# Performance work log

Hardware: AMD Instinct MI355X
Metric: run time of the kernel (lower is better)

The kernel has to match this reference:

```python
import jax, jax.numpy as jnp
import numpy as np

B, C, H, W = 8, 512, 32, 32
NH = 8
DH = C // NH
HW = H * W
LN_EPS = 1e-5
NORM_EPS = 1e-12  # torch F.normalize eps


def setup_inputs() -> dict:
    key = jax.random.key(0)
    ks = jax.random.split(key, 8)
    s = 0.02
    return {
        "x": jax.random.normal(ks[0], (B, C, H, W), dtype=jnp.float32),
        "qkv_w": jax.random.normal(ks[1], (3 * C, C), dtype=jnp.float32) * s,
        "proj_w": jax.random.normal(ks[2], (C, C), dtype=jnp.float32) * s,
        "proj_b": jnp.zeros((C,), dtype=jnp.float32),
        "temperature": jnp.ones((NH, 1, 1), dtype=jnp.float32),
        "ln_g": jnp.ones((C,), dtype=jnp.float32),
        "ln_b": jnp.zeros((C,), dtype=jnp.float32),
        "pos_embed": jax.random.normal(ks[3], (1, HW, C), dtype=jnp.float32) * s,
        "dw_w": jax.random.normal(ks[4], (C, 1, 3, 3), dtype=jnp.float32) * s,
        "dw_b": jnp.zeros((C,), dtype=jnp.float32),
        "pw_w": jax.random.normal(ks[5], (C, C, 1, 1), dtype=jnp.float32) * s,
        "pw_b": jnp.zeros((C,), dtype=jnp.float32),
    }


def _l2norm_tokens(t):
    # normalize along token axis (dim=-2), like F.normalize(t, dim=-2)
    n = jnp.sqrt(jnp.sum(t * t, axis=-2, keepdims=True))
    return t / jnp.maximum(n, NORM_EPS)


def _layernorm(t, g, b):
    mu = jnp.mean(t, axis=-1, keepdims=True)
    var = jnp.mean((t - mu) ** 2, axis=-1, keepdims=True)
    return (t - mu) * jax.lax.rsqrt(var + LN_EPS) * g + b


def _dsconv(t, dw_w, dw_b, pw_w, pw_b):
    # depthwise 3x3 SAME + pointwise 1x1, NCHW / OIHW
    y = jax.lax.conv_general_dilated(
        t, dw_w, window_strides=(1, 1), padding="SAME",
        dimension_numbers=("NCHW", "OIHW", "NCHW"), feature_group_count=C)
    y = y + dw_b[None, :, None, None]
    y = jax.lax.conv_general_dilated(
        y, pw_w, window_strides=(1, 1), padding="SAME",
        dimension_numbers=("NCHW", "OIHW", "NCHW"))
    return y + pw_b[None, :, None, None]


def reference(x, qkv_w, proj_w, proj_b, temperature, ln_g, ln_b, pos_embed, dw_w, dw_b, pw_w, pw_b):
    save = x
    t = jnp.transpose(x.reshape(B, C, HW), (0, 2, 1))  # [B, HW, C]
    t = t + pos_embed
    # qkv projection (no bias)
    qkv = t @ qkv_w.T  # [B, HW, 3C]
    qkv = qkv.reshape(B, HW, 3, NH, DH).transpose(2, 0, 3, 1, 4)  # [3,B,NH,HW,DH]
    q, k, v = qkv[0], qkv[1], qkv[2]
    q = _l2norm_tokens(q)
    k = _l2norm_tokens(k)
    attn = jnp.einsum("bhnd,bhmd->bhnm", q, k) * temperature[None]  # [B,NH,HW,HW]
    attn = jax.nn.softmax(attn, axis=-1)
    o = jnp.einsum("bhnm,bhmd->bhnd", attn, v)  # [B,NH,HW,DH]
    o = o.transpose(0, 2, 1, 3).reshape(B, HW, C)
    o = o @ proj_w.T + proj_b
    o = _layernorm(o, ln_g, ln_b)
    o = jnp.transpose(o, (0, 2, 1)).reshape(B, C, H, W)
    o = o + save
    return o + _dsconv(o, dw_w, dw_b, pw_w, pw_b)
```

## Files before the change

kernel.cpp:

```cpp
#include <hip/hip_runtime.h>
#include <math.h>

#define BB_ 8
#define C_ 512
#define C3_ 1536
#define HW_ 1024
#define NH_ 8
#define DH_ 64
#define HH_ 32
#define WW_ 32

typedef __attribute__((ext_vector_type(8))) short short8;
typedef __attribute__((ext_vector_type(4))) short short4v;
typedef __attribute__((ext_vector_type(8))) unsigned short ushort8;
typedef __attribute__((ext_vector_type(4))) unsigned short ushort4_t;
typedef __attribute__((ext_vector_type(4))) float f32x4;
typedef unsigned short ushort;

__device__ inline ushort f2bf(float f) {
  union { float f; unsigned u; } v;
  v.f = f;
  unsigned r = v.u + 0x7fffu + ((v.u >> 16) & 1u);
  return (ushort)(r >> 16);
}
__device__ inline float bf2f(ushort u) {
  union { unsigned u; float f; } v;
  v.u = ((unsigned)u) << 16;
  return v.f;
}

#define GLD16(gptr, lptr)                                                     \
  __builtin_amdgcn_global_load_lds(                                           \
      (const __attribute__((address_space(1))) unsigned int*)(gptr),          \
      (__attribute__((address_space(3))) unsigned int*)(lptr), 16, 0, 0)

__device__ inline f32x4 pv_mfma(const ushort* vp, short4v pf, f32x4 acc) {
#if __has_builtin(__builtin_amdgcn_mfma_f32_16x16x16_bf16)
  short4v vf = *(const short4v*)vp;
  return __builtin_amdgcn_mfma_f32_16x16x16_bf16(vf, pf, acc, 0, 0, 0);
#elif __has_builtin(__builtin_amdgcn_mfma_f32_16x16x16bf16_1k)
  short4v vf = *(const short4v*)vp;
  return __builtin_amdgcn_mfma_f32_16x16x16bf16_1k(vf, pf, acc, 0, 0, 0);
#else
  short4v v4 = *(const short4v*)vp;
  short8 vf = {v4[0], v4[1], v4[2], v4[3], 0, 0, 0, 0};
  short8 pf8 = {pf[0], pf[1], pf[2], pf[3], 0, 0, 0, 0};
  return __builtin_amdgcn_mfma_f32_16x16x32_bf16(vf, pf8, acc, 0, 0, 0);
#endif
}

__global__ void cvt_weights_kernel(const float* __restrict__ qkv_w,
                                   const float* __restrict__ proj_w,
                                   const float* __restrict__ pw_w,
                                   ushort* __restrict__ dst) {
  int i = blockIdx.x * 256 + threadIdx.x;
  if (i < 786432) dst[i] = f2bf(qkv_w[i]);
  else if (i < 1048576) dst[i] = f2bf(proj_w[i - 786432]);
  else dst[i] = f2bf(pw_w[i - 1048576]);
}

__global__ __launch_bounds__(256) void add_pos_kernel(
    const float* __restrict__ x, const float* __restrict__ pos,
    ushort* __restrict__ t, ushort* __restrict__ xT) {
  __shared__ float tile[64][65];
  const int tid = threadIdx.x;
  const int n0 = blockIdx.x * 64, c0 = blockIdx.y * 64, b = blockIdx.z;
#pragma unroll
  for (int it = 0; it < 4; it++) {
    int c_l = (tid >> 4) + it * 16;
    int n_l4 = (tid & 15) * 4;
    float4 v = *(const float4*)&x[((size_t)(b * C_ + c0 + c_l)) * HW_ + n0 + n_l4];
    tile[c_l][n_l4 + 0] = v.x;
    tile[c_l][n_l4 + 1] = v.y;
    tile[c_l][n_l4 + 2] = v.z;
    tile[c_l][n_l4 + 3] = v.w;
  }
  __syncthreads();
#pragma unroll
  for (int it = 0; it < 4; it++) {
    int n_l = (tid >> 4) + it * 16;
    int c_l4 = (tid & 15) * 4;
    size_t token = (size_t)(b * HW_ + n0 + n_l);
    float4 pv = *(const float4*)&pos[(n0 + n_l) * C_ + c0 + c_l4];
    float xv0 = tile[c_l4 + 0][n_l], xv1 = tile[c_l4 + 1][n_l];
    float xv2 = tile[c_l4 + 2][n_l], xv3 = tile[c_l4 + 3][n_l];
    ushort4_t tb = {f2bf(xv0 + pv.x), f2bf(xv1 + pv.y), f2bf(xv2 + pv.z),
                    f2bf(xv3 + pv.w)};
    ushort4_t xb = {f2bf(xv0), f2bf(xv1), f2bf(xv2), f2bf(xv3)};
    *(ushort4_t*)&t[token * C_ + c0 + c_l4] = tb;
    *(ushort4_t*)&xT[token * C_ + c0 + c_l4] = xb;
  }
}

__global__ __launch_bounds__(256) void gemm_128(
    const ushort* __restrict__ A, const ushort* __restrict__ Wm,
    ushort* __restrict__ out, int N, int K) {
  __shared__ alignas(16) ushort As[128 * 32];
  __shared__ alignas(16) ushort Bs[128 * 32];
  const int bn = blockIdx.x * 128, bm = blockIdx.y * 128;
  const int tid = threadIdx.x;
  const int w = tid >> 6, lane = tid & 63;
  const int wm = 64 * (w & 1), wn = 64 * (w >> 1);
  const int l15 = lane & 15, lq = lane >> 4;

  f32x4 acc[4][4];
#pragma unroll
  for (int i = 0; i < 4; i++)
#pragma unroll
    for (int j = 0; j < 4; j++) acc[i][j] = (f32x4){0.f, 0.f, 0.f, 0.f};

  const int srr = lane >> 2, sq1 = lane & 3;

  for (int k0 = 0; k0 < K; k0 += 32) {
    __syncthreads();
#pragma unroll
    for (int j = 0; j < 2; j++) {
      int r = 32 * w + 16 * j + srr;
      int q = (sq1 - (r >> 1)) & 3;
      GLD16(A + (size_t)(bm + r) * K + k0 + q * 8, &As[(32 * w + 16 * j) * 32]);
      GLD16(Wm + (size_t)(bn + r) * K + k0 + q * 8, &Bs[(32 * w + 16 * j) * 32]);
    }
    __syncthreads();
    short8 af[4], bf[4];
#pragma unroll
    for (int nt = 0; nt < 4; nt++) {
      int r = wm + nt * 16 + l15;
      af[nt] = *(const short8*)&As[r * 32 + (((lq + (r >> 1)) & 3) * 8)];
      int c = wn + nt * 16 + l15;
      bf[nt] = *(const short8*)&Bs[c * 32 + (((lq + (c >> 1)) & 3) * 8)];
    }
#pragma unroll
    for (int i = 0; i < 4; i++)
#pragma unroll
      for (int j = 0; j < 4; j++)
        acc[i][j] = __builtin_amdgcn_mfma_f32_16x16x32_bf16(af[i], bf[j],
                                                            acc[i][j], 0, 0, 0);
  }

#pragma unroll
  for (int i = 0; i < 4; i++) {
#pragma unroll
    for (int j = 0; j < 4; j++) {
      int c = bn + wn + j * 16 + l15;
#pragma unroll
      for (int r = 0; r < 4; r++) {
        int m = bm + wm + i * 16 + lq * 4 + r;
        out[(size_t)m * N + c] = f2bf(acc[i][j][r]);
      }
    }
  }
}

template <int EPI>
__global__ __launch_bounds__(256) void gemm_n64(
    const ushort* __restrict__ A, const ushort* __restrict__ Wm,
    const float* __restrict__ bias, float* __restrict__ out,
    const float* __restrict__ resid, int N, int K) {
  __shared__ alignas(16) ushort As[128 * 32];
  __shared__ alignas(16) ushort Bs[64 * 32];
  const int bn = blockIdx.x * 64, bm = blockIdx.y * 128;
  const int tid = threadIdx.x;
  const int w = tid >> 6, lane = tid & 63;
  const int wm = 64 * (w & 1), wn = 32 * (w >> 1);
  const int l15 = lane & 15, lq = lane >> 4;

  f32x4 acc[4][2];
#pragma unroll
  for (int i = 0; i < 4; i++)
#pragma unroll
    for (int j = 0; j < 2; j++) acc[i][j] = (f32x4){0.f, 0.f, 0.f, 0.f};

  const int srr = lane >> 2, sq1 = lane & 3;

  for (int k0 = 0; k0 < K; k0 += 32) {
    __syncthreads();
#pragma unroll
    for (int j = 0; j < 2; j++) {
      int r = 32 * w + 16 * j + srr;
      int q = (sq1 - (r >> 1)) & 3;
      GLD16(A + (size_t)(bm + r) * K + k0 + q * 8, &As[(32 * w + 16 * j) * 32]);
    }
    {
      int r = 16 * w + srr;
      int q = (sq1 - (r >> 1)) & 3;
      GLD16(Wm + (size_t)(bn + r) * K + k0 + q * 8, &Bs[(16 * w) * 32]);
    }
    __syncthreads();
    short8 af[4], bf[2];
#pragma unroll
    for (int nt = 0; nt < 4; nt++) {
      int r = wm + nt * 16 + l15;
      af[nt] = *(const short8*)&As[r * 32 + (((lq + (r >> 1)) & 3) * 8)];
    }
#pragma unroll
    for (int j = 0; j < 2; j++) {
      int c = wn + j * 16 + l15;
      bf[j] = *(const short8*)&Bs[c * 32 + (((lq + (c >> 1)) & 3) * 8)];
    }
#pragma unroll
    for (int i = 0; i < 4; i++)
#pragma unroll
      for (int j = 0; j < 2; j++)
        acc[i][j] = __builtin_amdgcn_mfma_f32_16x16x32_bf16(af[i], bf[j],
                                                            acc[i][j], 0, 0, 0);
  }

#pragma unroll
  for (int i = 0; i < 4; i++) {
#pragma unroll
    for (int j = 0; j < 2; j++) {
      int c = bn + wn + j * 16 + l15;
      float bv = bias[c];
#pragma unroll
      for (int r = 0; r < 4; r++) {
        int m = bm + wm + i * 16 + lq * 4 + r;
        float v = acc[i][j][r] + bv;
        if (EPI == 1) {
          out[(size_t)m * N + c] = v;
        } else {
          int b = m >> 10, s = m & (HW_ - 1);
          out[((size_t)(b * C_ + c)) * HW_ + s] = v + resid[(size_t)m * C_ + c];
        }
      }
    }
  }
}

__global__ __launch_bounds__(256) void vt_kernel(const ushort* __restrict__ qkv,
                                                 ushort* __restrict__ vt) {
  __shared__ ushort tileT[64][72];
  const int bh = blockIdx.x >> 2, seg = blockIdx.x & 3;
  const int b = bh >> 3, h = bh & 7;
  const int tid = threadIdx.x;
  const ushort* src = qkv + (size_t)b * HW_ * C3_ + 2 * C_ + h * 64;
  for (int t = 0; t < 4; t++) {
    int n0 = seg * 256 + t * 64;
    __syncthreads();
#pragma unroll
    for (int it = 0; it < 2; it++) {
      int row = it * 32 + (tid >> 3);
      int c8 = (tid & 7) * 8;
      ushort8 v = *(const ushort8*)&src[(size_t)(n0 + row) * C3_ + c8];
#pragma unroll
      for (int j = 0; j < 8; j++) tileT[c8 + j][row] = v[j];
    }
    __syncthreads();
#pragma unroll
    for (int it = 0; it < 2; it++) {
      int d = it * 32 + (tid >> 3);
      int nch = (tid & 7) * 8;
      ushort8 o8 = *(const ushort8*)&tileT[d][nch];
      *(ushort8*)&vt[((size_t)(bh * 64 + d)) * HW_ + n0 + nch] = o8;
    }
  }
}

__global__ __launch_bounds__(256) void qk_norms_stage1(
    const ushort* __restrict__ qkv, float* __restrict__ partials) {
  __shared__ float smq[32][65], smk[32][65];
  const int blk = blockIdx.x;
  const int bh = blk >> 3, seg = blk & 7;
  const int b = bh >> 3, h = bh & 7;
  const int tid = threadIdx.x;
  const int trow = tid >> 3, chunk = tid & 7;
  float sq[8] = {}, sk[8] = {};
  const ushort* base = qkv + (size_t)b * HW_ * C3_ + h * 64 + chunk * 8;
#pragma unroll
  for (int i = 0; i < 4; i++) {
    int n = seg * 128 + i * 32 + trow;
    const ushort* p = base + (size_t)n * C3_;
    ushort8 q8 = *(const ushort8*)p;
    ushort8 k8 = *(const ushort8*)(p + C_);
#pragma unroll
    for (int j = 0; j < 8; j++) {
      float qv = bf2f(q8[j]), kv = bf2f(k8[j]);
      sq[j] += qv * qv;
      sk[j] += kv * kv;
    }
  }
#pragma unroll
  for (int j = 0; j < 8; j++) {
    smq[trow][chunk * 8 + j] = sq[j];
    smk[trow][chunk * 8 + j] = sk[j];
  }
  __syncthreads();
  if (tid < 64) {
    float s = 0.f;
    for (int i = 0; i < 32; i++) s += smq[i][tid];
    partials[((size_t)(bh * 8 + seg) * 2 + 0) * 64 + tid] = s;
  } else if (tid < 128) {
    int d = tid - 64;
    float s = 0.f;
    for (int i = 0; i < 32; i++) s += smk[i][d];
    partials[((size_t)(bh * 8 + seg) * 2 + 1) * 64 + d] = s;
  }
}

__global__ void qk_norms_stage2(const float* __restrict__ partials,
                                float* __restrict__ invq,
                                float* __restrict__ invk) {
  const int bh = blockIdx.x;
  const int tid = threadIdx.x;
  const int which = tid >> 6, d = tid & 63;
  float s = 0.f;
#pragma unroll
  for (int seg = 0; seg < 8; seg++)
    s += partials[((size_t)(bh * 8 + seg) * 2 + which) * 64 + d];
  float r = 1.0f / fmaxf(sqrtf(s), 1e-12f);
  if (which == 0) invq[bh * 64 + d] = r;
  else invk[bh * 64 + d] = r;
}

__global__ __launch_bounds__(512) void attn_mfma_kernel(
    const ushort* __restrict__ qkv, const ushort* __restrict__ vt,
    const float* __restrict__ invq, const float* __restrict__ invk,
    const float* __restrict__ temp, ushort* __restrict__ o) {
  __shared__ alignas(16) ushort Ks[64 * 64];
  __shared__ alignas(16) ushort Vts[64 * 64];

  const int tid = threadIdx.x;
  const int w = tid >> 6, lane = tid & 63;
  const int quad = lane >> 4, lcol = lane & 15;
  const int bh = blockIdx.x >> 3;
  const int qt = blockIdx.x & 7;
  const int b = bh >> 3, h = bh & 7;
  const int q0 = qt * 128;

  short8 qf[2];
  {
    const int m = q0 + w * 16 + lcol;
    const ushort* qrow = qkv + ((size_t)(b * HW_ + m)) * C3_ + h * 64;
    const float tmp = temp[h];
#pragma unroll
    for (int kc = 0; kc < 2; kc++) {
      union { short8 v; ushort u[8]; } pk;
#pragma unroll
      for (int j = 0; j < 8; j++) {
        int d = kc * 32 + quad * 8 + j;
        float s = invq[bh * 64 + d] * invk[bh * 64 + d] * tmp;
        pk.u[j] = f2bf(bf2f(qrow[d]) * s);
      }
      qf[kc] = pk.v;
    }
  }

  f32x4 ot[4];
#pragma unroll
  for (int dt = 0; dt < 4; dt++) ot[dt] = (f32x4){0.f, 0.f, 0.f, 0.f};
  float lsum = 0.f;

  const ushort* kg = qkv + (size_t)b * HW_ * C3_ + C_ + h * 64;
  const ushort* vg = vt + (size_t)(bh * 64) * HW_;

  const int srow = tid >> 3;
  const int sc = tid & 7;
  const int scg = sc ^ (srow & 7);

  for (int kt = 0; kt < 16; kt++) {
    __syncthreads();
    GLD16(kg + (size_t)(kt * 64 + srow) * C3_ + scg * 8, &Ks[w * 512]);
    GLD16(vg + (size_t)srow * HW_ + kt * 64 + scg * 8, &Vts[w * 512]);
    __syncthreads();

    f32x4 sfr[4];
#pragma unroll
    for (int nt = 0; nt < 4; nt++) sfr[nt] = (f32x4){0.f, 0.f, 0.f, 0.f};
#pragma unroll
    for (int kc = 0; kc < 2; kc++) {
#pragma unroll
      for (int nt = 0; nt < 4; nt++) {
        int row = nt * 16 + lcol;
        short8 kf = *(const short8*)
            &Ks[row * 64 + (((kc * 4 + quad) ^ (row & 7)) * 8)];
        sfr[nt] =
            __builtin_amdgcn_mfma_f32_16x16x32_bf16(kf, qf[kc], sfr[nt], 0, 0, 0);
      }
    }

    ushort pk[4][4];
#pragma unroll
    for (int nt = 0; nt < 4; nt++) {
#pragma unroll
      for (int r = 0; r < 4; r++) {
        float e = __expf(sfr[nt][r]);
        lsum += e;
        pk[nt][r] = f2bf(e);
      }
    }

#pragma unroll
    for (int nt = 0; nt < 4; nt++) {
      short4v pf = {(short)pk[nt][0], (short)pk[nt][1], (short)pk[nt][2],
                    (short)pk[nt][3]};
      int key = nt * 16 + quad * 4;
#pragma unroll
      for (int dt = 0; dt < 4; dt++) {
        int d = dt * 16 + lcol;
        const ushort* vp =
            &Vts[d * 64 + (((key >> 3) ^ (d & 7)) * 8) + (key & 7)];
        ot[dt] = pv_mfma(vp, pf, ot[dt]);
      }
    }
  }

  lsum += __shfl_xor(lsum, 16);
  lsum += __shfl_xor(lsum, 32);
  const float inv = 1.0f / lsum;

  const int m = q0 + w * 16 + lcol;
  ushort* orow = o + ((size_t)(b * HW_ + m)) * C_ + h * 64;
#pragma unroll
  for (int dt = 0; dt < 4; dt++) {
    ushort4_t pkb = {f2bf(ot[dt][0] * inv), f2bf(ot[dt][1] * inv),
                     f2bf(ot[dt][2] * inv), f2bf(ot[dt][3] * inv)};
    *(ushort4_t*)&orow[dt * 16 + quad * 4] = pkb;
  }
}

__global__ void ln_residual_kernel(float* __restrict__ po, const ushort* xT,
                                   const float* __restrict__ g,
                                   const float* __restrict__ bb, ushort* ybf) {
  int token = blockIdx.x;
  int t = threadIdx.x;
  float* row = po + (size_t)token * C_;
  float v0 = row[t], v1 = row[t + 256];
  float s = v0 + v1;
#pragma unroll
  for (int off = 32; off; off >>= 1) s += __shfl_xor(s, off);
  __shared__ float wr[4];
  if ((t & 63) == 0) wr[t >> 6] = s;
  __syncthreads();
  float mu = (wr[0] + wr[1] + wr[2] + wr[3]) * (1.0f / C_);
  float d0 = v0 - mu, d1 = v1 - mu;
  float vs = d0 * d0 + d1 * d1;
#pragma unroll
  for (int off = 32; off; off >>= 1) vs += __shfl_xor(vs, off);
  __syncthreads();
  if ((t & 63) == 0) wr[t >> 6] = vs;
  __syncthreads();
  float var = (wr[0] + wr[1] + wr[2] + wr[3]) * (1.0f / C_);
  float rstd = rsqrtf(var + 1e-5f);
  float r0 = bf2f(xT[(size_t)token * C_ + t]);
  float r1 = bf2f(xT[(size_t)token * C_ + t + 256]);
  float o0 = d0 * rstd * g[t] + bb[t] + r0;
  float o1 = d1 * rstd * g[t + 256] + bb[t + 256] + r1;
  row[t] = o0;
  row[t + 256] = o1;
  ybf[(size_t)token * C_ + t] = f2bf(o0);
  ybf[(size_t)token * C_ + t + 256] = f2bf(o1);
}

__global__ __launch_bounds__(256) void dwconv_kernel(
    const ushort* __restrict__ y, const float* __restrict__ w,
    const float* __restrict__ bias, ushort* __restrict__ out) {
  const int cg = threadIdx.x & 63, tg = threadIdx.x >> 6;
  const int c0 = cg * 8;
  float wreg[9][8], breg[8];
#pragma unroll
  for (int j = 0; j < 8; j++) {
    breg[j] = bias[c0 + j];
#pragma unroll
    for (int kk = 0; kk < 9; kk++) wreg[kk][j] = w[(c0 + j) * 9 + kk];
  }
  for (int i = 0; i < 4; i++) {
    int token = blockIdx.x * 16 + tg * 4 + i;
    int b = token >> 10, s = token & (HW_ - 1);
    int hh = s >> 5, ww = s & 31;
    float acc[8];
#pragma unroll
    for (int j = 0; j < 8; j++) acc[j] = breg[j];
#pragma unroll
    for (int ky = 0; ky < 3; ky++) {
      int yy = hh + ky - 1;
      if (yy < 0 || yy >= HH_) continue;
#pragma unroll
      for (int kx = 0; kx < 3; kx++) {
        int xx = ww + kx - 1;
        if (xx < 0 || xx >= WW_) continue;
        ushort8 v8 = *(const ushort8*)
            &y[((size_t)(b * HW_ + yy * 32 + xx)) * C_ + c0];
        const float* wk = wreg[ky * 3 + kx];
#pragma unroll
        for (int j = 0; j < 8; j++) acc[j] += wk[j] * bf2f(v8[j]);
      }
    }
    ushort8 pk;
#pragma unroll
    for (int j = 0; j < 8; j++) pk[j] = f2bf(acc[j]);
    *(ushort8*)&out[(size_t)token * C_ + c0] = pk;
  }
}

extern "C" void kernel_launch(void* const* d_in, const int* in_sizes, int n_in,
                              void* d_out, int out_size, void* d_ws,
                              size_t ws_size, hipStream_t stream) {
  const float* x = (const float*)d_in[0];
  const float* qkv_w = (const float*)d_in[1];
  const float* proj_w = (const float*)d_in[2];
  const float* proj_b = (const float*)d_in[3];
  const float* temperature = (const float*)d_in[4];
  const float* ln_g = (const float*)d_in[5];
  const float* ln_b = (const float*)d_in[6];
  const float* pos = (const float*)d_in[7];
  const float* dw_w = (const float*)d_in[8];
  const float* dw_b = (const float*)d_in[9];
  const float* pw_w = (const float*)d_in[10];
  const float* pw_b = (const float*)d_in[11];
  float* out = (float*)d_out;

  float* ws = (float*)d_ws;
  ushort* qkv_bf = (ushort*)ws;
  ushort* t_bf = (ushort*)(ws + (size_t)6 * 1024 * 1024);
  float* proj_out = ws + (size_t)8 * 1024 * 1024;
  ushort* xT_bf = (ushort*)(ws + (size_t)12 * 1024 * 1024);
  ushort* wts = (ushort*)(ws + (size_t)14 * 1024 * 1024);
  ushort* qkvw_bf = wts;
  ushort* projw_bf = wts + 786432;
  ushort* pww_bf = wts + 1048576;
  float* invq = ws + (size_t)15 * 1024 * 1024;
  float* invk = invq + 512;
  float* partials = invk + 512;
  ushort* vtb = (ushort*)(ws + (size_t)16 * 1024 * 1024);

  const int M = BB_ * HW_;

  cvt_weights_kernel<<<1310720 / 256, 256, 0, stream>>>(qkv_w, proj_w, pw_w,
                                                        wts);
  add_pos_kernel<<<dim3(16, 8, 8), 256, 0, stream>>>(x, pos, t_bf, xT_bf);
  gemm_128<<<dim3(C3_ / 128, M / 128), 256, 0, stream>>>(t_bf, qkvw_bf,
                                                         qkv_bf, C3_, C_);
  vt_kernel<<<256, 256, 0, stream>>>(qkv_bf, vtb);
  qk_norms_stage1<<<512, 256, 0, stream>>>(qkv_bf, partials);
  qk_norms_stage2<<<64, 128, 0, stream>>>(partials, invq, invk);
  attn_mfma_kernel<<<BB_ * NH_ * (HW_ / 128), 512, 0, stream>>>(
      qkv_bf, vtb, invq, invk, temperature, t_bf);
  gemm_n64<1><<<dim3(C_ / 64, M / 128), 256, 0, stream>>>(
      t_bf, projw_bf, proj_b, proj_out, nullptr, C_, C_);
  ln_residual_kernel<<<M, 256, 0, stream>>>(proj_out, xT_bf, ln_g, ln_b,
                                            xT_bf);
  dwconv_kernel<<<M / 16, 256, 0, stream>>>(xT_bf, dw_w, dw_b, t_bf);
  gemm_n64<2><<<dim3(C_ / 64, M / 128), 256, 0, stream>>>(
      t_bf, pww_bf, pw_b, out, proj_out, C_, C_);
}
```

Baseline: 220.8 us.

## Fuse V-transpose and QK norm sums into QKV GEMM epilogue, merge prep kernels

The weight-conversion, pos-add and zeroing of the norm accumulators now run in one combined prep launch. The QKV GEMM epilogue accumulates per-channel squared sums for q and k with atomics, and writes V directly in transposed layout. This removes the separate vt and two norm kernels along with their extra reads of the qkv buffer. The projection output becomes bf16, the LayerNorm kernel is vectorised, and the final residual reads the bf16 LN output. Attention moves to 64-query tiles with 256 threads. The cost is float atomics, which make the sums order-nondeterministic, and lower precision on the projection output and residual.

```diff
diff --git a/kernel.cpp b/kernel.cpp
--- a/kernel.cpp
+++ b/kernel.cpp
@@ -49,22 +49,27 @@
 #endif
 }
 
-__global__ void cvt_weights_kernel(const float* __restrict__ qkv_w,
-                                   const float* __restrict__ proj_w,
-                                   const float* __restrict__ pw_w,
-                                   ushort* __restrict__ dst) {
-  int i = blockIdx.x * 256 + threadIdx.x;
-  if (i < 786432) dst[i] = f2bf(qkv_w[i]);
-  else if (i < 1048576) dst[i] = f2bf(proj_w[i - 786432]);
-  else dst[i] = f2bf(pw_w[i - 1048576]);
-}
-
-__global__ __launch_bounds__(256) void add_pos_kernel(
+__global__ __launch_bounds__(256) void prep_kernel(
     const float* __restrict__ x, const float* __restrict__ pos,
-    ushort* __restrict__ t, ushort* __restrict__ xT) {
+    const float* __restrict__ qkv_w, const float* __restrict__ proj_w,
+    const float* __restrict__ pw_w, ushort* __restrict__ t,
+    ushort* __restrict__ xT, ushort* __restrict__ wts,
+    float* __restrict__ sums) {
+  const int bid = blockIdx.x;
+  const int tid = threadIdx.x;
+  if (bid >= 6144) {
+    sums[(bid - 6144) * 256 + tid] = 0.f;
+    return;
+  }
+  if (bid >= 1024) {
+    int i = (bid - 1024) * 256 + tid;
+    if (i < 786432) wts[i] = f2bf(qkv_w[i]);
+    else if (i < 1048576) wts[i] = f2bf(proj_w[i - 786432]);
+    else wts[i] = f2bf(pw_w[i - 1048576]);
+    return;
+  }
   __shared__ float tile[64][65];
-  const int tid = threadIdx.x;
-  const int n0 = blockIdx.x * 64, c0 = blockIdx.y * 64, b = blockIdx.z;
+  const int n0 = (bid & 15) * 64, c0 = ((bid >> 4) & 7) * 64, b = bid >> 7;
 #pragma unroll
   for (int it = 0; it < 4; it++) {
     int c_l = (tid >> 4) + it * 16;
@@ -92,9 +97,11 @@
   }
 }
 
-__global__ __launch_bounds__(256) void gemm_128(
+__global__ __launch_bounds__(256) void gemm_qkv(
     const ushort* __restrict__ A, const ushort* __restrict__ Wm,
-    ushort* __restrict__ out, int N, int K) {
+    ushort* __restrict__ out, ushort* __restrict__ vt,
+    float* __restrict__ qsum, float* __restrict__ ksum) {
+  const int N = C3_, K = C_;
   __shared__ alignas(16) ushort As[128 * 32];
   __shared__ alignas(16) ushort Bs[128 * 32];
   const int bn = blockIdx.x * 128, bm = blockIdx.y * 128;
@@ -137,15 +144,41 @@
                                                             acc[i][j], 0, 0, 0);
   }
 
-#pragma unroll
-  for (int i = 0; i < 4; i++) {
+  const int b = bm >> 10;
+  if (bn < 1024) {
 #pragma unroll
     for (int j = 0; j < 4; j++) {
       int c = bn + wn + j * 16 + l15;
-#pragma unroll
-      for (int r = 0; r < 4; r++) {
-        int m = bm + wm + i * 16 + lq * 4 + r;
-        out[(size_t)m * N + c] = f2bf(acc[i][j][r]);
+      float ss = 0.f;
+#pragma unroll
+      for (int i = 0; i < 4; i++) {
+#pragma unroll
+        for (int r = 0; r < 4; r++) {
+          int m = bm + wm + i * 16 + lq * 4 + r;
+          float v = acc[i][j][r];
+          ss += v * v;
+          out[(size_t)m * N + c] = f2bf(v);
+        }
+      }
+      ss += __shfl_xor(ss, 16);
+      ss += __shfl_xor(ss, 32);
+      if (lq == 0) {
+        if (c < 512) atomicAdd(&qsum[b * 512 + c], ss);
+        else atomicAdd(&ksum[b * 512 + c - 512], ss);
+      }
+    }
+  } else {
+#pragma unroll
+    for (int j = 0; j < 4; j++) {
+      int c = bn + wn + j * 16 + l15;
+      int hd = c - 1024;
+      ushort* vrow = vt + ((size_t)(b * 512 + hd)) * HW_;
+#pragma unroll
+      for (int i = 0; i < 4; i++) {
+        int n0 = (bm & 1023) + wm + i * 16 + lq * 4;
+        ushort4_t pv = {f2bf(acc[i][j][0]), f2bf(acc[i][j][1]),
+                        f2bf(acc[i][j][2]), f2bf(acc[i][j][3])};
+        *(ushort4_t*)&vrow[n0] = pv;
       }
     }
   }
@@ -154,8 +187,8 @@
 template <int EPI>
 __global__ __launch_bounds__(256) void gemm_n64(
     const ushort* __restrict__ A, const ushort* __restrict__ Wm,
-    const float* __restrict__ bias, float* __restrict__ out,
-    const float* __restrict__ resid, int N, int K) {
+    const float* __restrict__ bias, void* __restrict__ outv,
+    const ushort* __restrict__ resid, int N, int K) {
   __shared__ alignas(16) ushort As[128 * 32];
   __shared__ alignas(16) ushort Bs[64 * 32];
   const int bn = blockIdx.x * 64, bm = blockIdx.y * 128;
@@ -216,129 +249,53 @@
         int m = bm + wm + i * 16 + lq * 4 + r;
         float v = acc[i][j][r] + bv;
         if (EPI == 1) {
-          out[(size_t)m * N + c] = v;
+          ((ushort*)outv)[(size_t)m * N + c] = f2bf(v);
         } else {
           int b = m >> 10, s = m & (HW_ - 1);
-          out[((size_t)(b * C_ + c)) * HW_ + s] = v + resid[(size_t)m * C_ + c];
+          ((float*)outv)[((size_t)(b * C_ + c)) * HW_ + s] =
+              v + bf2f(resid[(size_t)m * C_ + c]);
         }
       }
     }
   }
 }
 
-__global__ __launch_bounds__(256) void vt_kernel(const ushort* __restrict__ qkv,
-                                                 ushort* __restrict__ vt) {
-  __shared__ ushort tileT[64][72];
-  const int bh = blockIdx.x >> 2, seg = blockIdx.x & 3;
-  const int b = bh >> 3, h = bh & 7;
-  const int tid = threadIdx.x;
-  const ushort* src = qkv + (size_t)b * HW_ * C3_ + 2 * C_ + h * 64;
-  for (int t = 0; t < 4; t++) {
-    int n0 = seg * 256 + t * 64;
-    __syncthreads();
-#pragma unroll
-    for (int it = 0; it < 2; it++) {
-      int row = it * 32 + (tid >> 3);
-      int c8 = (tid & 7) * 8;
-      ushort8 v = *(const ushort8*)&src[(size_t)(n0 + row) * C3_ + c8];
-#pragma unroll
-      for (int j = 0; j < 8; j++) tileT[c8 + j][row] = v[j];
-    }
-    __syncthreads();
-#pragma unroll
-    for (int it = 0; it < 2; it++) {
-      int d = it * 32 + (tid >> 3);
-      int nch = (tid & 7) * 8;
-      ushort8 o8 = *(const ushort8*)&tileT[d][nch];
-      *(ushort8*)&vt[((size_t)(bh * 64 + d)) * HW_ + n0 + nch] = o8;
-    }
-  }
-}
-
-__global__ __launch_bounds__(256) void qk_norms_stage1(
-    const ushort* __restrict__ qkv, float* __restrict__ partials) {
-  __shared__ float smq[32][65], smk[32][65];
-  const int blk = blockIdx.x;
-  const int bh = blk >> 3, seg = blk & 7;
-  const int b = bh >> 3, h = bh & 7;
-  const int tid = threadIdx.x;
-  const int trow = tid >> 3, chunk = tid & 7;
-  float sq[8] = {}, sk[8] = {};
-  const ushort* base = qkv + (size_t)b * HW_ * C3_ + h * 64 + chunk * 8;
-#pragma unroll
-  for (int i = 0; i < 4; i++) {
-    int n = seg * 128 + i * 32 + trow;
-    const ushort* p = base + (size_t)n * C3_;
-    ushort8 q8 = *(const ushort8*)p;
-    ushort8 k8 = *(const ushort8*)(p + C_);
-#pragma unroll
-    for (int j = 0; j < 8; j++) {
-      float qv = bf2f(q8[j]), kv = bf2f(k8[j]);
-      sq[j] += qv * qv;
-      sk[j] += kv * kv;
-    }
-  }
-#pragma unroll
-  for (int j = 0; j < 8; j++) {
-    smq[trow][chunk * 8 + j] = sq[j];
-    smk[trow][chunk * 8 + j] = sk[j];
-  }
-  __syncthreads();
-  if (tid < 64) {
-    float s = 0.f;
-    for (int i = 0; i < 32; i++) s += smq[i][tid];
-    partials[((size_t)(bh * 8 + seg) * 2 + 0) * 64 + tid] = s;
-  } else if (tid < 128) {
-    int d = tid - 64;
-    float s = 0.f;
-    for (int i = 0; i < 32; i++) s += smk[i][d];
-    partials[((size_t)(bh * 8 + seg) * 2 + 1) * 64 + d] = s;
-  }
-}
-
-__global__ void qk_norms_stage2(const float* __restrict__ partials,
-                                float* __restrict__ invq,
-                                float* __restrict__ invk) {
-  const int bh = blockIdx.x;
-  const int tid = threadIdx.x;
-  const int which = tid >> 6, d = tid & 63;
-  float s = 0.f;
-#pragma unroll
-  for (int seg = 0; seg < 8; seg++)
-    s += partials[((size_t)(bh * 8 + seg) * 2 + which) * 64 + d];
-  float r = 1.0f / fmaxf(sqrtf(s), 1e-12f);
-  if (which == 0) invq[bh * 64 + d] = r;
-  else invk[bh * 64 + d] = r;
-}
-
-__global__ __launch_bounds__(512) void attn_mfma_kernel(
+__global__ __launch_bounds__(256) void attn_mfma_kernel(
     const ushort* __restrict__ qkv, const ushort* __restrict__ vt,
-    const float* __restrict__ invq, const float* __restrict__ invk,
+    const float* __restrict__ qsum, const float* __restrict__ ksum,
     const float* __restrict__ temp, ushort* __restrict__ o) {
   __shared__ alignas(16) ushort Ks[64 * 64];
   __shared__ alignas(16) ushort Vts[64 * 64];
+  __shared__ float sc_lds[64];
 
   const int tid = threadIdx.x;
   const int w = tid >> 6, lane = tid & 63;
   const int quad = lane >> 4, lcol = lane & 15;
-  const int bh = blockIdx.x >> 3;
-  const int qt = blockIdx.x & 7;
+  const int bh = blockIdx.x >> 4;
+  const int qt = blockIdx.x & 15;
   const int b = bh >> 3, h = bh & 7;
-  const int q0 = qt * 128;
+  const int q0 = qt * 64;
+
+  if (tid < 64) {
+    float qs = qsum[b * 512 + h * 64 + tid];
+    float ks = ksum[b * 512 + h * 64 + tid];
+    float iq = 1.0f / fmaxf(sqrtf(qs), 1e-12f);
+    float ik = 1.0f / fmaxf(sqrtf(ks), 1e-12f);
+    sc_lds[tid] = iq * ik * temp[h];
+  }
+  __syncthreads();
 
   short8 qf[2];
   {
     const int m = q0 + w * 16 + lcol;
     const ushort* qrow = qkv + ((size_t)(b * HW_ + m)) * C3_ + h * 64;
-    const float tmp = temp[h];
 #pragma unroll
     for (int kc = 0; kc < 2; kc++) {
       union { short8 v; ushort u[8]; } pk;
 #pragma unroll
       for (int j = 0; j < 8; j++) {
         int d = kc * 32 + quad * 8 + j;
-        float s = invq[bh * 64 + d] * invk[bh * 64 + d] * tmp;
-        pk.u[j] = f2bf(bf2f(qrow[d]) * s);
+        pk.u[j] = f2bf(bf2f(qrow[d]) * sc_lds[d]);
       }
       qf[kc] = pk.v;
     }
@@ -352,14 +309,20 @@
   const ushort* kg = qkv + (size_t)b * HW_ * C3_ + C_ + h * 64;
   const ushort* vg = vt + (size_t)(bh * 64) * HW_;
 
-  const int srow = tid >> 3;
+  const int srow0 = tid >> 3;
   const int sc = tid & 7;
-  const int scg = sc ^ (srow & 7);
 
   for (int kt = 0; kt < 16; kt++) {
     __syncthreads();
-    GLD16(kg + (size_t)(kt * 64 + srow) * C3_ + scg * 8, &Ks[w * 512]);
-    GLD16(vg + (size_t)srow * HW_ + kt * 64 + scg * 8, &Vts[w * 512]);
+#pragma unroll
+    for (int it = 0; it < 2; it++) {
+      int row = srow0 + it * 32;
+      int scg = sc ^ (row & 7);
+      GLD16(kg + (size_t)(kt * 64 + row) * C3_ + scg * 8,
+            &Ks[w * 512 + it * 2048]);
+      GLD16(vg + (size_t)row * HW_ + kt * 64 + scg * 8,
+            &Vts[w * 512 + it * 2048]);
+    }
     __syncthreads();
 
     f32x4 sfr[4];
@@ -417,13 +380,14 @@
   }
 }
 
-__global__ void ln_residual_kernel(float* __restrict__ po, const ushort* xT,
+__global__ void ln_residual_kernel(const ushort* __restrict__ po,
+                                   const ushort* xT,
                                    const float* __restrict__ g,
                                    const float* __restrict__ bb, ushort* ybf) {
   int token = blockIdx.x;
   int t = threadIdx.x;
-  float* row = po + (size_t)token * C_;
-  float v0 = row[t], v1 = row[t + 256];
+  const unsigned pv = *(const unsigned*)&po[(size_t)token * C_ + 2 * t];
+  float v0 = bf2f((ushort)(pv & 0xffff)), v1 = bf2f((ushort)(pv >> 16));
   float s = v0 + v1;
 #pragma unroll
   for (int off = 32; off; off >>= 1) s += __shfl_xor(s, off);
@@ -440,14 +404,11 @@
   __syncthreads();
   float var = (wr[0] + wr[1] + wr[2] + wr[3]) * (1.0f / C_);
   float rstd = rsqrtf(var + 1e-5f);
-  float r0 = bf2f(xT[(size_t)token * C_ + t]);
-  float r1 = bf2f(xT[(size_t)token * C_ + t + 256]);
-  float o0 = d0 * rstd * g[t] + bb[t] + r0;
-  float o1 = d1 * rstd * g[t + 256] + bb[t + 256] + r1;
-  row[t] = o0;
-  row[t + 256] = o1;
-  ybf[(size_t)token * C_ + t] = f2bf(o0);
-  ybf[(size_t)token * C_ + t + 256] = f2bf(o1);
+  const unsigned rv = *(const unsigned*)&xT[(size_t)token * C_ + 2 * t];
+  float o0 = d0 * rstd * g[2 * t] + bb[2 * t] + bf2f((ushort)(rv & 0xffff));
+  float o1 = d1 * rstd * g[2 * t + 1] + bb[2 * t + 1] + bf2f((ushort)(rv >> 16));
+  unsigned ov = (unsigned)f2bf(o0) | ((unsigned)f2bf(o1) << 16);
+  *(unsigned*)&ybf[(size_t)token * C_ + 2 * t] = ov;
 }
 
 __global__ __launch_bounds__(256) void dwconv_kernel(
@@ -511,34 +472,30 @@
   float* ws = (float*)d_ws;
   ushort* qkv_bf = (ushort*)ws;
   ushort* t_bf = (ushort*)(ws + (size_t)6 * 1024 * 1024);
-  float* proj_out = ws + (size_t)8 * 1024 * 1024;
+  ushort* proj_bf = (ushort*)(ws + (size_t)8 * 1024 * 1024);
   ushort* xT_bf = (ushort*)(ws + (size_t)12 * 1024 * 1024);
   ushort* wts = (ushort*)(ws + (size_t)14 * 1024 * 1024);
   ushort* qkvw_bf = wts;
   ushort* projw_bf = wts + 786432;
   ushort* pww_bf = wts + 1048576;
-  float* invq = ws + (size_t)15 * 1024 * 1024;
-  float* invk = invq + 512;
-  float* partials = invk + 512;
+  float* sums = ws + (size_t)15 * 1024 * 1024;
+  float* qsum = sums;
+  float* ksum = sums + 4096;
   ushort* vtb = (ushort*)(ws + (size_t)16 * 1024 * 1024);
 
   const int M = BB_ * HW_;
 
-  cvt_weights_kernel<<<1310720 / 256, 256, 0, stream>>>(qkv_w, proj_w, pw_w,
-                                                        wts);
-  add_pos_kernel<<<dim3(16, 8, 8), 256, 0, stream>>>(x, pos, t_bf, xT_bf);
-  gemm_128<<<dim3(C3_ / 128, M / 128), 256, 0, stream>>>(t_bf, qkvw_bf,
-                                                         qkv_bf, C3_, C_);
-  vt_kernel<<<256, 256, 0, stream>>>(qkv_bf, vtb);
-  qk_norms_stage1<<<512, 256, 0, stream>>>(qkv_bf, partials);
-  qk_norms_stage2<<<64, 128, 0, stream>>>(partials, invq, invk);
-  attn_mfma_kernel<<<BB_ * NH_ * (HW_ / 128), 512, 0, stream>>>(
-      qkv_bf, vtb, invq, invk, temperature, t_bf);
+  prep_kernel<<<6176, 256, 0, stream>>>(x, pos, qkv_w, proj_w, pw_w, t_bf,
+                                        xT_bf, wts, sums);
+  gemm_qkv<<<dim3(C3_ / 128, M / 128), 256, 0, stream>>>(
+      t_bf, qkvw_bf, qkv_bf, vtb, qsum, ksum);
+  attn_mfma_kernel<<<BB_ * NH_ * (HW_ / 64), 256, 0, stream>>>(
+      qkv_bf, vtb, qsum, ksum, temperature, t_bf);
   gemm_n64<1><<<dim3(C_ / 64, M / 128), 256, 0, stream>>>(
-      t_bf, projw_bf, proj_b, proj_out, nullptr, C_, C_);
-  ln_residual_kernel<<<M, 256, 0, stream>>>(proj_out, xT_bf, ln_g, ln_b,
+      t_bf, projw_bf, proj_b, proj_bf, nullptr, C_, C_);
+  ln_residual_kernel<<<M, 256, 0, stream>>>(proj_bf, xT_bf, ln_g, ln_b,
                                             xT_bf);
   dwconv_kernel<<<M / 16, 256, 0, stream>>>(xT_bf, dw_w, dw_b, t_bf);
   gemm_n64<2><<<dim3(C_ / 64, M / 128), 256, 0, stream>>>(
-      t_bf, pww_bf, pw_b, out, proj_out, C_, C_);
-}
+      t_bf, pww_bf, pw_b, out, xT_bf, C_, C_);
+}
```

Result: faster. 213.8 us (-3.2%).
